# Kernel optimization log

Hardware: AMD Instinct MI355X
Metric: run time of the kernel (lower is better)

Reference implementation:

```python
import jax, jax.numpy as jnp
import numpy as np

N_NODES = 10000
N_EDGES = 160000
IN_CH = 1030
HID = 256
HEADS = 4
OUT_CH = 49
NEG_SLOPE = 0.2
EPS = 1e-5


def setup_inputs() -> dict:
    key = jax.random.key(0)
    ks = jax.random.split(key, 20)
    HC = HID * HEADS  # 1024
    inp = {
        "x": jax.random.normal(ks[0], (N_NODES, IN_CH), dtype=jnp.float32),
        "edge_index": jax.random.randint(ks[1], (2, N_EDGES), 0, N_NODES, dtype=jnp.int64),
        # conv1 (GATv2): lin_l (source), lin_r (target), att, out bias
        "c1_wl": jax.random.normal(ks[2], (IN_CH, HC), dtype=jnp.float32) * 0.03,
        "c1_bl": jnp.zeros((HC,), dtype=jnp.float32),
        "c1_wr": jax.random.normal(ks[3], (IN_CH, HC), dtype=jnp.float32) * 0.03,
        "c1_br": jnp.zeros((HC,), dtype=jnp.float32),
        "c1_att": jax.random.normal(ks[4], (HEADS, HID), dtype=jnp.float32) * 0.06,
        "c1_bias": jnp.zeros((HC,), dtype=jnp.float32),
        # norm1 (per-node LayerNorm over channels)
        "ln1_w": jnp.ones((HC,), dtype=jnp.float32),
        "ln1_b": jnp.zeros((HC,), dtype=jnp.float32),
        # conv2
        "c2_wl": jax.random.normal(ks[5], (HC, HC), dtype=jnp.float32) * 0.03,
        "c2_bl": jnp.zeros((HC,), dtype=jnp.float32),
        "c2_wr": jax.random.normal(ks[6], (HC, HC), dtype=jnp.float32) * 0.03,
        "c2_br": jnp.zeros((HC,), dtype=jnp.float32),
        "c2_att": jax.random.normal(ks[7], (HEADS, HID), dtype=jnp.float32) * 0.06,
        "c2_bias": jnp.zeros((HC,), dtype=jnp.float32),
        # norm2
        "ln2_w": jnp.ones((HC,), dtype=jnp.float32),
        "ln2_b": jnp.zeros((HC,), dtype=jnp.float32),
        # classifier: Linear(HC, HID) -> ELU -> Linear(HID, OUT_CH)
        "cls_w1": jax.random.normal(ks[8], (HC, HID), dtype=jnp.float32) * 0.03,
        "cls_b1": jnp.zeros((HID,), dtype=jnp.float32),
        "cls_w2": jax.random.normal(ks[9], (HID, OUT_CH), dtype=jnp.float32) * 0.06,
        "cls_b2": jnp.zeros((OUT_CH,), dtype=jnp.float32),
    }
    return inp


def gatv2_conv(x, src, dst, wl, bl, wr, br, att, bias, n_nodes):
    """PyG GATv2Conv, concat heads. src/dst include self loops."""
    H, C = att.shape
    xl = (x @ wl + bl).reshape(-1, H, C)  # source transform [N,H,C]
    xr = (x @ wr + br).reshape(-1, H, C)  # target transform [N,H,C]
    m = xl[src] + xr[dst]                  # [E,H,C] gather + add
    e = jnp.einsum("ehc,hc->eh", jax.nn.leaky_relu(m, NEG_SLOPE), att)  # [E,H]
    # segment softmax over destination node
    emax = jax.ops.segment_max(e, dst, num_segments=n_nodes)
    p = jnp.exp(e - emax[dst])
    denom = jax.ops.segment_sum(p, dst, num_segments=n_nodes)
    alpha = p / (denom[dst] + 1e-16)       # [E,H]
    out = jax.ops.segment_sum(xl[src] * alpha[:, :, None], dst, num_segments=n_nodes)
    return out.reshape(n_nodes, H * C) + bias


def layer_norm(x, w, b):
    mu = jnp.mean(x, axis=-1, keepdims=True)
    var = jnp.var(x, axis=-1, keepdims=True)
    return (x - mu) / jnp.sqrt(var + EPS) * w + b


def reference(x, edge_index, c1_wl, c1_bl, c1_wr, c1_br, c1_att, c1_bias,
              ln1_w, ln1_b, c2_wl, c2_bl, c2_wr, c2_br, c2_att, c2_bias,
              ln2_w, ln2_b, cls_w1, cls_b1, cls_w2, cls_b2):
    n = x.shape[0]
    loops = jnp.arange(n, dtype=edge_index.dtype)
    src = jnp.concatenate([edge_index[0], loops])  # add_self_loops=True
    dst = jnp.concatenate([edge_index[1], loops])

    h = gatv2_conv(x, src, dst, c1_wl, c1_bl, c1_wr, c1_br, c1_att, c1_bias, n)
    h = jax.nn.elu(layer_norm(h, ln1_w, ln1_b))
    # dropout: identity at inference
    h = gatv2_conv(h, src, dst, c2_wl, c2_bl, c2_wr, c2_br, c2_att, c2_bias, n)
    h = jax.nn.elu(layer_norm(h, ln2_w, ln2_b))
    h = jax.nn.elu(h @ cls_w1 + cls_b1)
    return h @ cls_w2 + cls_b2  # [N, 49]
```

## Files before the change

### kernel.cpp

```cpp
#include <hip/hip_runtime.h>
#include <stdint.h>

#define N_NODES 10000
#define N_EDGES 160000
#define E_TOT   170000
#define IN_CH   1030
#define HC      1024
#define OUT_CH  49
#define NEG_SLOPE 0.2f
#define LN_EPS 1e-5f
#define LOG2E 1.4426950408889634f

#define MPAD  10112
#define K1PAD 1088

typedef __attribute__((ext_vector_type(8))) __bf16 bf16x8;
typedef __attribute__((ext_vector_type(8))) _Float16 h8;
typedef __attribute__((ext_vector_type(4))) float floatx4;
typedef __attribute__((ext_vector_type(2))) float floatx2;
typedef _Float16 h2 __attribute__((ext_vector_type(2)));

static __device__ __forceinline__ unsigned short f2bf(float f) {
  union { float f; uint32_t u; } v; v.f = f;
  uint32_t u = v.u;
  u += 0x7fffu + ((u >> 16) & 1u);
  return (unsigned short)(u >> 16);
}
static __device__ __forceinline__ unsigned short f2h(float f) {
  _Float16 h = (_Float16)f;
  union { _Float16 h; unsigned short u; } v; v.h = h; return v.u;
}
static __device__ __forceinline__ h2 bits2h2(uint32_t u) {
  union { uint32_t i; h2 h; } v; v.i = u; return v.h;
}
static __device__ __forceinline__ floatx2 h2f2(h2 a) {
  floatx2 r; r.x = (float)a.x; r.y = (float)a.y; return r;
}

static __device__ __forceinline__ float wred_add(float x) {
#define DPP_ADD(ctrl, rmask)                                                   \
  x += __builtin_bit_cast(float, __builtin_amdgcn_update_dpp(                  \
           0, __builtin_bit_cast(int, x), ctrl, rmask, 0xf, true))
  DPP_ADD(0x111, 0xf);
  DPP_ADD(0x112, 0xf);
  DPP_ADD(0x114, 0xf);
  DPP_ADD(0x118, 0xf);
  DPP_ADD(0x142, 0xa);
  DPP_ADD(0x143, 0xc);
#undef DPP_ADD
  return __builtin_bit_cast(float,
      __builtin_amdgcn_readlane(__builtin_bit_cast(int, x), 63));
}


__global__ void cast_x_kernel(const float* __restrict__ x, unsigned short* __restrict__ xa,
                              int* __restrict__ counts) {
  int idx = blockIdx.x * 256 + threadIdx.x;
  if (idx < N_NODES) counts[idx] = 0;
  if (idx >= N_NODES * (K1PAD / 4)) return;
  int m = idx / (K1PAD / 4), k4 = idx - m * (K1PAD / 4);
  int k = k4 * 4;
  ushort4 o;
  if (k + 3 < IN_CH) {
    float2 v0 = *(const float2*)(x + (size_t)m * IN_CH + k);
    float2 v1 = *(const float2*)(x + (size_t)m * IN_CH + k + 2);
    o.x = f2bf(v0.x); o.y = f2bf(v0.y); o.z = f2bf(v1.x); o.w = f2bf(v1.y);
  } else {
    o.x = (k     < IN_CH) ? f2bf(x[(size_t)m * IN_CH + k    ]) : (unsigned short)0;
    o.y = (k + 1 < IN_CH) ? f2bf(x[(size_t)m * IN_CH + k + 1]) : (unsigned short)0;
    o.z = (k + 2 < IN_CH) ? f2bf(x[(size_t)m * IN_CH + k + 2]) : (unsigned short)0;
    o.w = (unsigned short)0;
  }
  *(ushort4*)(xa + (size_t)m * K1PAD + k) = o;
}

static __device__ __forceinline__ void transpose_body(
    float (*tile)[33], const float* __restrict__ wa, const float* __restrict__ wb,
    int split, int lda, int ldb, int Kvalid, int Kout,
    unsigned short* __restrict__ out, int bx, int by, int t, bool f16o) {
  int n0 = bx * 32, k0 = by * 32;
  int tx = t & 31, ty = t >> 5;
#pragma unroll
  for (int i = 0; i < 4; i++) {
    int k = k0 + ty + i * 8;
    int n = n0 + tx;
    float v = 0.f;
    if (k < Kvalid) {
      if (n < split) v = wa[(size_t)k * lda + n];
      else if (ldb)  v = wb[(size_t)k * ldb + (n - split)];
    }
    tile[ty + i * 8][tx] = v;
  }
  __syncthreads();
#pragma unroll
  for (int i = 0; i < 4; i++) {
    int n = n0 + ty + i * 8;
    int k = k0 + tx;
    float v = tile[tx][ty + i * 8];
    out[(size_t)n * Kout + k] = f16o ? f2h(v) : f2bf(v);
  }
}

#define NB_W1 2176
#define NB_W2 2048
#define NB_WC 256
#define NB_WC2 16
#define NB_CNT 665
__global__ __launch_bounds__(256) void prep2_kernel(
    const float* __restrict__ c1_wl, const float* __restrict__ c1_wr,
    const float* __restrict__ c2_wl, const float* __restrict__ c2_wr,
    const float* __restrict__ cls_w1, const float* __restrict__ cls_w2,
    const int* __restrict__ dstArr, int* __restrict__ counts,
    unsigned short* __restrict__ wt1, unsigned short* __restrict__ wt2,
    unsigned short* __restrict__ wtc1, unsigned short* __restrict__ wtc2)
{
  __shared__ float tile[32][33];
  int b = blockIdx.x, t = threadIdx.x;
  if (b < NB_W1) {
    transpose_body(tile, c1_wl, c1_wr, 1024, 1024, 1024, IN_CH, K1PAD, wt1, b & 63, b >> 6, t, false);
  } else if (b < NB_W1 + NB_W2) {
    int bb = b - NB_W1;
    transpose_body(tile, c2_wl, c2_wr, 1024, 1024, 1024, 1024, 1024, wt2, bb & 63, bb >> 6, t, false);
  } else if (b < NB_W1 + NB_W2 + NB_WC) {
    int bb = b - (NB_W1 + NB_W2);
    transpose_body(tile, cls_w1, cls_w1, 256, 256, 256, 1024, 1024, wtc1, bb & 7, bb >> 3, t, false);
  } else if (b < NB_W1 + NB_W2 + NB_WC + NB_WC2) {
    int bb = b - (NB_W1 + NB_W2 + NB_WC);
    transpose_body(tile, cls_w2, cls_w2, OUT_CH, OUT_CH, 0, 256, 256, wtc2, bb & 1, bb >> 1, t, true);
  } else {
    int e = (b - (NB_W1 + NB_W2 + NB_WC + NB_WC2)) * 256 + t;
    if (e < E_TOT) {
      int d = (e < N_EDGES) ? dstArr[e] : (e - N_EDGES);
      atomicAdd(&counts[d], 1);
    }
  }
}

__global__ __launch_bounds__(256) void scan_kernel(const int* __restrict__ counts,
                                                   int* __restrict__ rstart,
                                                   int* __restrict__ rwork) {
  __shared__ int sm[256];
  int t = threadIdx.x;
  int b0 = t * 40;
  int b1 = b0 + 40; if (b1 > N_NODES) b1 = N_NODES; if (b0 > N_NODES) b0 = N_NODES;
  int s = 0;
  for (int i = b0; i < b1; i++) s += counts[i];
  sm[t] = s; __syncthreads();
  for (int st = 1; st < 256; st <<= 1) {
    int add = (t >= st) ? sm[t - st] : 0;
    __syncthreads();
    sm[t] += add;
    __syncthreads();
  }
  int run = sm[t] - s;
  for (int i = b0; i < b1; i++) { rstart[i] = run; rwork[i] = run; run += counts[i]; }
  if (t == 255) rstart[N_NODES] = run;
}

__global__ void scatter_kernel(const int* __restrict__ srcArr, const int* __restrict__ dstArr,
                               int* __restrict__ rwork, int* __restrict__ csrsrc) {
  int e = blockIdx.x * 256 + threadIdx.x;
  if (e >= E_TOT) return;
  if (e < 16) csrsrc[E_TOT + e] = 0;
  int d, sv;
  if (e < N_EDGES) { d = dstArr[e]; sv = srcArr[e]; }
  else { d = e - N_EDGES; sv = d; }
  int pos = atomicAdd(&rwork[d], 1);
  csrsrc[pos] = sv;
}

template <int MODE, int KC>
__global__ __launch_bounds__(256, 4) void gemm_bf16(
    const unsigned short* __restrict__ A, const unsigned short* __restrict__ Bt,
    float* __restrict__ Cf, unsigned short* __restrict__ Cb,
    const float* __restrict__ blo, const float* __restrict__ bhi,
    int M, int ldc, int bsplit)
{
  __shared__ __align__(16) unsigned short As[128 * 64];
  __shared__ __align__(16) unsigned short Bs[128 * 64];
  const int t = threadIdx.x;
  const int w = t >> 6, lane = t & 63;

  const unsigned int nwg = gridDim.x * gridDim.y;
  const unsigned int bid = blockIdx.y * gridDim.x + blockIdx.x;
  const unsigned int q8 = nwg >> 3, r8 = nwg & 7;
  const unsigned int xcd = bid & 7, sub = bid >> 3;
  const unsigned int wg = (xcd < r8 ? xcd * (q8 + 1) : r8 * (q8 + 1) + (xcd - r8) * q8) + sub;
  const int tile_n = (wg % gridDim.x) * 128, tile_m = (wg / gridDim.x) * 128;

  floatx4 acc[4][4] = {};

  const int qq = w * 64 + lane;
  const int row0 = qq >> 3;
  const int gj = (qq & 7) ^ (row0 & 7);
  const unsigned short* gA0 = A  + (size_t)(tile_m + row0) * KC + gj * 8;
  const unsigned short* gB0 = Bt + (size_t)(tile_n + row0) * KC + gj * 8;

  const int wm = (w >> 1) * 64, wn = (w & 1) * 64;
  const int lrow = lane & 15, cg0 = (lane >> 4);
  const int sw = lrow & 7;

#pragma unroll 1
  for (int k0 = 0; k0 < KC; k0 += 64) {
#pragma unroll
    for (int p = 0; p < 4; p++) {
      __builtin_amdgcn_global_load_lds(
          (const __attribute__((address_space(1))) void*)(gA0 + p * 32 * KC),
          (__attribute__((address_space(3))) void*)(As + p * 2048 + w * 512), 16, 0, 0);
      __builtin_amdgcn_global_load_lds(
          (const __attribute__((address_space(1))) void*)(gB0 + p * 32 * KC),
          (__attribute__((address_space(3))) void*)(Bs + p * 2048 + w * 512), 16, 0, 0);
    }
    gA0 += 64; gB0 += 64;
    __syncthreads();
#pragma unroll
    for (int h = 0; h < 2; h++) {
      const int sc = (h * 4 + cg0) ^ sw;
      bf16x8 a[4], b[4];
#pragma unroll
      for (int mi = 0; mi < 4; mi++)
        a[mi] = *(const bf16x8*)(As + (wm + mi * 16 + lrow) * 64 + sc * 8);
#pragma unroll
      for (int ni = 0; ni < 4; ni++)
        b[ni] = *(const bf16x8*)(Bs + (wn + ni * 16 + lrow) * 64 + sc * 8);
#pragma unroll
      for (int mi = 0; mi < 4; mi++)
#pragma unroll
        for (int ni = 0; ni < 4; ni++)
          acc[mi][ni] = __builtin_amdgcn_mfma_f32_16x16x32_bf16(a[mi], b[ni], acc[mi][ni], 0, 0, 0);
    }
    __syncthreads();
  }

  float bcol[4];
#pragma unroll
  for (int ni = 0; ni < 4; ni++) {
    int n = tile_n + wn + ni * 16 + lrow;
    bcol[ni] = (n < bsplit) ? blo[n] : bhi[n - bsplit];
  }

  const int rbase = (lane >> 4) * 4;
#pragma unroll
  for (int mi = 0; mi < 4; mi++) {
#pragma unroll
    for (int r = 0; r < 4; r++) {
      int m = tile_m + wm + mi * 16 + rbase + r;
      if (m >= M) continue;
#pragma unroll
      for (int ni = 0; ni < 4; ni++) {
        int n = tile_n + wn + ni * 16 + lrow;
        float v = acc[mi][ni][r] + bcol[ni];
        if (MODE == 0) {
          Cf[(size_t)m * ldc + n] = v;
        } else if (MODE == 1) {
          Cf[(size_t)m * ldc + n] = v > 0.f ? v : expm1f(v);
        } else {
          Cb[(size_t)m * 2048 + n] = f2h(v);
        }
      }
    }
  }
}


__global__ __launch_bounds__(256) void gat_ln_kernel(
    const unsigned short* __restrict__ xlr,
    const float* __restrict__ att,
    const int* __restrict__ csrsrc, const int* __restrict__ rstart,
    const float* __restrict__ bias,
    const float* __restrict__ lnw, const float* __restrict__ lnb,
    unsigned short* __restrict__ out)
{
  const int d = blockIdx.x;
  const int t = threadIdx.x;
  const int lane = t & 63, wv = t >> 6;
  const int c = wv * 256 + lane * 4;

  uint2 xru = *(const uint2*)(xlr + (size_t)d * 2048 + 1024 + c);
  h2 xr0 = bits2h2(xru.x), xr1 = bits2h2(xru.y);
  float4 aw4 = *(const float4*)(att + c);
  h2 aw0, aw1;
  aw0.x = (_Float16)(aw4.x * LOG2E); aw0.y = (_Float16)(aw4.y * LOG2E);
  aw1.x = (_Float16)(aw4.z * LOG2E); aw1.y = (_Float16)(aw4.w * LOG2E);
  const h2 ns = {(_Float16)NEG_SLOPE, (_Float16)NEG_SLOPE};
  const unsigned short* xbase = xlr + c;

  int start = rstart[d], deg = rstart[d + 1] - start;

  float m = -3.0e38f, l = 0.f;
  floatx2 accA = {0.f, 0.f}, accB = {0.f, 0.f};

  int i = 0;
  if (deg >= 4) {
    int sA0 = csrsrc[start],     sA1 = csrsrc[start + 1];
    int sA2 = csrsrc[start + 2], sA3 = csrsrc[start + 3];
    uint2 uA0 = *(const uint2*)(xbase + (size_t)sA0 * 2048);
    uint2 uA1 = *(const uint2*)(xbase + (size_t)sA1 * 2048);
    uint2 uA2 = *(const uint2*)(xbase + (size_t)sA2 * 2048);
    uint2 uA3 = *(const uint2*)(xbase + (size_t)sA3 * 2048);
    int sB0 = csrsrc[start + 4], sB1 = csrsrc[start + 5];
    int sB2 = csrsrc[start + 6], sB3 = csrsrc[start + 7];
    for (; i + 4 <= deg; i += 4) {
      int sC0 = csrsrc[start + i + 8],  sC1 = csrsrc[start + i + 9];
      int sC2 = csrsrc[start + i + 10], sC3 = csrsrc[start + i + 11];
      uint2 uB0 = *(const uint2*)(xbase + (size_t)sB0 * 2048);
      uint2 uB1 = *(const uint2*)(xbase + (size_t)sB1 * 2048);
      uint2 uB2 = *(const uint2*)(xbase + (size_t)sB2 * 2048);
      uint2 uB3 = *(const uint2*)(xbase + (size_t)sB3 * 2048);

      h2 xh0a = bits2h2(uA0.x), xh0b = bits2h2(uA0.y);
      h2 xh1a = bits2h2(uA1.x), xh1b = bits2h2(uA1.y);
      h2 xh2a = bits2h2(uA2.x), xh2b = bits2h2(uA2.y);
      h2 xh3a = bits2h2(uA3.x), xh3b = bits2h2(uA3.y);
      h2 t0a = xh0a + xr0, t0b = xh0b + xr1;
      h2 t1a = xh1a + xr0, t1b = xh1b + xr1;
      h2 t2a = xh2a + xr0, t2b = xh2b + xr1;
      h2 t3a = xh3a + xr0, t3b = xh3b + xr1;
      h2 r0a = __builtin_elementwise_max(t0a, t0a * ns);
      h2 r0b = __builtin_elementwise_max(t0b, t0b * ns);
      h2 r1a = __builtin_elementwise_max(t1a, t1a * ns);
      h2 r1b = __builtin_elementwise_max(t1b, t1b * ns);
      h2 r2a = __builtin_elementwise_max(t2a, t2a * ns);
      h2 r2b = __builtin_elementwise_max(t2b, t2b * ns);
      h2 r3a = __builtin_elementwise_max(t3a, t3a * ns);
      h2 r3b = __builtin_elementwise_max(t3b, t3b * ns);
      float p0 = __builtin_amdgcn_fdot2(r0b, aw1, __builtin_amdgcn_fdot2(r0a, aw0, 0.f, false), false);
      float p1 = __builtin_amdgcn_fdot2(r1b, aw1, __builtin_amdgcn_fdot2(r1a, aw0, 0.f, false), false);
      float p2 = __builtin_amdgcn_fdot2(r2b, aw1, __builtin_amdgcn_fdot2(r2a, aw0, 0.f, false), false);
      float p3 = __builtin_amdgcn_fdot2(r3b, aw1, __builtin_amdgcn_fdot2(r3a, aw0, 0.f, false), false);
      p0 = wred_add(p0);
      p1 = wred_add(p1);
      p2 = wred_add(p2);
      p3 = wred_add(p3);
      float mx = fmaxf(fmaxf(p0, p1), fmaxf(p2, p3));
      if (mx > m) {
        float sc = exp2f(m - mx);
        floatx2 scv; scv.x = sc; scv.y = sc;
        accA *= scv; accB *= scv; l *= sc;
        m = mx;
      }
      float pe0 = exp2f(p0 - m), pe1 = exp2f(p1 - m);
      float pe2 = exp2f(p2 - m), pe3 = exp2f(p3 - m);
      floatx2 x0A = h2f2(xh0a), x0B = h2f2(xh0b);
      floatx2 x1A = h2f2(xh1a), x1B = h2f2(xh1b);
      floatx2 x2A = h2f2(xh2a), x2B = h2f2(xh2b);
      floatx2 x3A = h2f2(xh3a), x3B = h2f2(xh3b);
      floatx2 v0; v0.x = pe0; v0.y = pe0;
      floatx2 v1; v1.x = pe1; v1.y = pe1;
      floatx2 v2; v2.x = pe2; v2.y = pe2;
      floatx2 v3; v3.x = pe3; v3.y = pe3;
      accA += x0A * v0; accA += x1A * v1; accA += x2A * v2; accA += x3A * v3;
      accB += x0B * v0; accB += x1B * v1; accB += x2B * v2; accB += x3B * v3;
      l += pe0 + pe1 + pe2 + pe3;

      uA0 = uB0; uA1 = uB1; uA2 = uB2; uA3 = uB3;
      sB0 = sC0; sB1 = sC1; sB2 = sC2; sB3 = sC3;
    }
  }
  for (; i < deg; i++) {
    int s0 = csrsrc[start + i];
    uint2 u0 = *(const uint2*)(xbase + (size_t)s0 * 2048);
    h2 xh0a = bits2h2(u0.x), xh0b = bits2h2(u0.y);
    h2 t0a = xh0a + xr0, t0b = xh0b + xr1;
    h2 r0a = __builtin_elementwise_max(t0a, t0a * ns);
    h2 r0b = __builtin_elementwise_max(t0b, t0b * ns);
    float p0 = __builtin_amdgcn_fdot2(r0b, aw1, __builtin_amdgcn_fdot2(r0a, aw0, 0.f, false), false);
    p0 = wred_add(p0);
    if (p0 > m) {
      float sc = exp2f(m - p0);
      floatx2 scv; scv.x = sc; scv.y = sc;
      accA *= scv; accB *= scv; l *= sc;
      m = p0;
    }
    float pe0 = exp2f(p0 - m);
    floatx2 x0A = h2f2(xh0a), x0B = h2f2(xh0b);
    floatx2 pe0v; pe0v.x = pe0; pe0v.y = pe0;
    accA += x0A * pe0v;
    accB += x0B * pe0v;
    l += pe0;
  }

  float rd = 1.f / (l + 1e-16f);
  float4 bv = *(const float4*)(bias + c);
  float o0 = accA.x * rd + bv.x, o1 = accA.y * rd + bv.y;
  float o2 = accB.x * rd + bv.z, o3 = accB.y * rd + bv.w;

  __shared__ float ws1[4], ws2[4];
  float s1 = o0 + o1 + o2 + o3;
  float s2 = o0 * o0 + o1 * o1 + o2 * o2 + o3 * o3;
#pragma unroll
  for (int mm = 32; mm >= 1; mm >>= 1) {
    s1 += __shfl_xor(s1, mm, 64);
    s2 += __shfl_xor(s2, mm, 64);
  }
  if (lane == 0) { ws1[wv] = s1; ws2[wv] = s2; }
  __syncthreads();
  float mean = (ws1[0] + ws1[1] + ws1[2] + ws1[3]) * (1.f / 1024.f);
  float var  = (ws2[0] + ws2[1] + ws2[2] + ws2[3]) * (1.f / 1024.f) - mean * mean;
  float rstd = rsqrtf(var + LN_EPS);
  float4 wv4 = *(const float4*)(lnw + c);
  float4 bb  = *(const float4*)(lnb + c);
  float z0 = (o0 - mean) * rstd * wv4.x + bb.x; z0 = z0 > 0.f ? z0 : expm1f(z0);
  float z1 = (o1 - mean) * rstd * wv4.y + bb.y; z1 = z1 > 0.f ? z1 : expm1f(z1);
  float z2 = (o2 - mean) * rstd * wv4.z + bb.z; z2 = z2 > 0.f ? z2 : expm1f(z2);
  float z3 = (o3 - mean) * rstd * wv4.w + bb.w; z3 = z3 > 0.f ? z3 : expm1f(z3);
  ushort4 u;
  u.x = f2bf(z0); u.y = f2bf(z1); u.z = f2bf(z2); u.w = f2bf(z3);
  *(ushort4*)(out + (size_t)d * 1024 + c) = u;
}


extern __shared__ unsigned short clssm[];

__global__ __launch_bounds__(256) void cls_fused_kernel(
    const unsigned short* __restrict__ A,
    const unsigned short* __restrict__ Bt,
    const float* __restrict__ b1,
    const unsigned short* __restrict__ w2t,
    const float* __restrict__ b2,
    float* __restrict__ out)
{
  unsigned short* As = clssm;
  unsigned short* Bs = clssm + 8192;
  unsigned short* hbuf = clssm;

  const int t = threadIdx.x;
  const int w = t >> 6, lane = t & 63;
  const int tile_m = blockIdx.x * 128;

  const int q = w * 64 + lane;
  const int row0 = q >> 3;
  const int gj = (q & 7) ^ (row0 & 7);
  const unsigned short* gA0 = A  + (size_t)(tile_m + row0) * 1024 + gj * 8;
  const unsigned short* gB0 = Bt + (size_t)row0 * 1024 + gj * 8;

  const int wm = (w >> 1) * 64, wn = (w & 1) * 128;
  const int lrow = lane & 15, cg0 = lane >> 4, sw = lrow & 7;

  floatx4 acc[4][8] = {};

#pragma unroll 1
  for (int k0 = 0; k0 < 1024; k0 += 64) {
#pragma unroll
    for (int p = 0; p < 4; p++)
      __builtin_amdgcn_global_load_lds(
          (const __attribute__((address_space(1))) void*)(gA0 + p * 32 * 1024),
          (__attribute__((address_space(3))) void*)(As + p * 2048 + w * 512), 16, 0, 0);
#pragma unroll
    for (int s = 0; s < 8; s++)
      __builtin_amdgcn_global_load_lds(
          (const __attribute__((address_space(1))) void*)(gB0 + s * 32 * 1024),
          (__attribute__((address_space(3))) void*)(Bs + s * 2048 + w * 512), 16, 0, 0);
    gA0 += 64; gB0 += 64;
    __syncthreads();
#pragma unroll
    for (int h = 0; h < 2; h++) {
      const int sc = ((h << 2) | cg0) ^ sw;
      bf16x8 a[4], b[8];
#pragma unroll
      for (int mi = 0; mi < 4; mi++) {
        int ar = wm + mi * 16 + lrow;
        a[mi] = *(const bf16x8*)(As + (ar >> 5) * 2048 + (ar & 31) * 64 + sc * 8);
      }
#pragma unroll
      for (int ni = 0; ni < 8; ni++) {
        int br = wn + ni * 16 + lrow;
        b[ni] = *(const bf16x8*)(Bs + (br >> 5) * 2048 + (br & 31) * 64 + sc * 8);
      }
#pragma unroll
      for (int mi = 0; mi < 4; mi++)
#pragma unroll
        for (int ni = 0; ni < 8; ni++)
          acc[mi][ni] = __builtin_amdgcn_mfma_f32_16x16x32_bf16(a[mi], b[ni], acc[mi][ni], 0, 0, 0);
    }
    __syncthreads();
  }

  float bcol[8];
#pragma unroll
  for (int ni = 0; ni < 8; ni++) bcol[ni] = b1[wn + ni * 16 + lrow];
  const int rbase = cg0 * 4;
#pragma unroll
  for (int mi = 0; mi < 4; mi++) {
#pragma unroll
    for (int r = 0; r < 4; r++) {
      int row = wm + mi * 16 + rbase + r;
#pragma unroll
      for (int ni = 0; ni < 8; ni++) {
        int col = wn + ni * 16 + lrow;
        float v = acc[mi][ni][r] + bcol[ni];
        v = v > 0.f ? v : expm1f(v);
        int kc = (col >> 3) ^ (row & 7);
        hbuf[row * 256 + kc * 8 + (col & 7)] = f2h(v);
      }
    }
  }
  __syncthreads();

  floatx4 acc3[2][4] = {};
#pragma unroll
  for (int kst = 0; kst < 8; kst++) {
    h8 a3[2], b3[4];
#pragma unroll
    for (int mi = 0; mi < 2; mi++) {
      int ar = w * 32 + mi * 16 + lrow;
      int kc = (kst * 4 + cg0) ^ (ar & 7);
      a3[mi] = *(const h8*)(hbuf + ar * 256 + kc * 8);
    }
#pragma unroll
    for (int ni = 0; ni < 4; ni++) {
      int br = ni * 16 + lrow;
      b3[ni] = *(const h8*)(w2t + br * 256 + kst * 32 + cg0 * 8);
    }
#pragma unroll
    for (int mi = 0; mi < 2; mi++)
#pragma unroll
      for (int ni = 0; ni < 4; ni++)
        acc3[mi][ni] = __builtin_amdgcn_mfma_f32_16x16x32_f16(a3[mi], b3[ni], acc3[mi][ni], 0, 0, 0);
  }
#pragma unroll
  for (int mi = 0; mi < 2; mi++) {
    int rb = tile_m + w * 32 + mi * 16 + rbase;
#pragma unroll
    for (int r = 0; r < 4; r++) {
      int node = rb + r;
      if (node >= N_NODES) continue;
#pragma unroll
      for (int ni = 0; ni < 4; ni++) {
        int j = ni * 16 + lrow;
        if (j < OUT_CH) out[(size_t)node * OUT_CH + j] = acc3[mi][ni][r] + b2[j];
      }
    }
  }
}


extern "C" void kernel_launch(void* const* d_in, const int* in_sizes, int n_in,
                              void* d_out, int out_size, void* d_ws, size_t ws_size,
                              hipStream_t stream)
{
  const float* x       = (const float*)d_in[0];
  const int*   ei      = (const int*)d_in[1];
  const float* c1_wl   = (const float*)d_in[2];
  const float* c1_bl   = (const float*)d_in[3];
  const float* c1_wr   = (const float*)d_in[4];
  const float* c1_br   = (const float*)d_in[5];
  const float* c1_att  = (const float*)d_in[6];
  const float* c1_bias = (const float*)d_in[7];
  const float* ln1_w   = (const float*)d_in[8];
  const float* ln1_b   = (const float*)d_in[9];
  const float* c2_wl   = (const float*)d_in[10];
  const float* c2_bl   = (const float*)d_in[11];
  const float* c2_wr   = (const float*)d_in[12];
  const float* c2_br   = (const float*)d_in[13];
  const float* c2_att  = (const float*)d_in[14];
  const float* c2_bias = (const float*)d_in[15];
  const float* ln2_w   = (const float*)d_in[16];
  const float* ln2_b   = (const float*)d_in[17];
  const float* cls_w1  = (const float*)d_in[18];
  const float* cls_b1  = (const float*)d_in[19];
  const float* cls_w2  = (const float*)d_in[20];
  const float* cls_b2  = (const float*)d_in[21];

  const int* srcArr = ei;
  const int* dstArr = ei + N_EDGES;

  char* ws = (char*)d_ws;
  size_t off = 0;
  auto alloc = [&](size_t bytes) { void* p = ws + off; off += (bytes + 255) & ~(size_t)255; return p; };
  unsigned short* xa      = (unsigned short*)alloc((size_t)MPAD * K1PAD * 2);
  unsigned short* wt1     = (unsigned short*)alloc((size_t)2048 * K1PAD * 2);
  unsigned short* wt2     = (unsigned short*)alloc((size_t)2048 * 1024 * 2);
  unsigned short* wtc1    = (unsigned short*)alloc((size_t)256 * 1024 * 2);
  unsigned short* wtc2    = (unsigned short*)alloc((size_t)64 * 256 * 2);
  unsigned short* xlr     = (unsigned short*)alloc((size_t)N_NODES * 2048 * 2);
  unsigned short* hb      = (unsigned short*)alloc((size_t)MPAD * 1024 * 2);
  int*            counts  = (int*)alloc(N_NODES * 4);
  int*            rwork   = (int*)alloc(N_NODES * 4);
  int*            rstart  = (int*)alloc((N_NODES + 1) * 4);
  int*            csrsrc  = (int*)alloc((E_TOT + 16) * 4);
  (void)in_sizes; (void)n_in; (void)out_size; (void)ws_size;

  cast_x_kernel<<<(N_NODES * (K1PAD / 4) + 255) / 256, 256, 0, stream>>>(x, xa, counts);
  prep2_kernel<<<NB_W1 + NB_W2 + NB_WC + NB_WC2 + NB_CNT, 256, 0, stream>>>(
      c1_wl, c1_wr, c2_wl, c2_wr, cls_w1, cls_w2, dstArr, counts, wt1, wt2, wtc1, wtc2);

  scan_kernel<<<1, 256, 0, stream>>>(counts, rstart, rwork);
  scatter_kernel<<<(E_TOT + 255) / 256, 256, 0, stream>>>(srcArr, dstArr, rwork, csrsrc);

  gemm_bf16<2, K1PAD><<<dim3(16, 79), 256, 0, stream>>>(xa, wt1, nullptr, xlr, c1_bl, c1_br, N_NODES, 0, 1024);
  gat_ln_kernel<<<N_NODES, 256, 0, stream>>>(xlr, c1_att, csrsrc, rstart, c1_bias, ln1_w, ln1_b, hb);

  gemm_bf16<2, 1024><<<dim3(16, 79), 256, 0, stream>>>(hb, wt2, nullptr, xlr, c2_bl, c2_br, N_NODES, 0, 1024);
  gat_ln_kernel<<<N_NODES, 256, 0, stream>>>(xlr, c2_att, csrsrc, rstart, c2_bias, ln2_w, ln2_b, hb);

  cls_fused_kernel<<<79, 256, 65536, stream>>>(hb, wtc1, cls_b1, wtc2, cls_b2, (float*)d_out);
}
```

Baseline: 450.8 us.

## Widen GEMM tile to 256x128 with 512-thread workgroups

Replaces the 128x128, 256-thread bf16 GEMM with a 256x128 tile computed by 8 waves, so each B tile loaded into LDS serves twice as many rows. The grid shrinks to 640 workgroups and uses a simplified XCD-aware remap hardcoded to 80 blocks per XCD. Padded A buffers grow to 10240 rows to cover the larger M tiles. The aim is to cut global-to-LDS traffic per MFMA, at the cost of more LDS per block and possibly lower occupancy or less balanced waves.

```diff
diff --git a/kernel.cpp b/kernel.cpp
--- a/kernel.cpp
+++ b/kernel.cpp
@@ -12,6 +12,7 @@
 #define LOG2E 1.4426950408889634f
 
 #define MPAD  10112
+#define MPAD2 10240
 #define K1PAD 1088
 
 typedef __attribute__((ext_vector_type(8))) __bf16 bf16x8;
@@ -169,60 +170,59 @@
   csrsrc[pos] = sv;
 }
 
-template <int MODE, int KC>
-__global__ __launch_bounds__(256, 4) void gemm_bf16(
-    const unsigned short* __restrict__ A, const unsigned short* __restrict__ Bt,
-    float* __restrict__ Cf, unsigned short* __restrict__ Cb,
-    const float* __restrict__ blo, const float* __restrict__ bhi,
-    int M, int ldc, int bsplit)
+
+template <int KC>
+__global__ __launch_bounds__(512, 6) void gemm_wide(
+    const unsigned short* __restrict__ A,
+    const unsigned short* __restrict__ Bt,
+    unsigned short* __restrict__ Cb,
+    const float* __restrict__ blo, const float* __restrict__ bhi, int M)
 {
-  __shared__ __align__(16) unsigned short As[128 * 64];
+  __shared__ __align__(16) unsigned short As[256 * 64];
   __shared__ __align__(16) unsigned short Bs[128 * 64];
   const int t = threadIdx.x;
   const int w = t >> 6, lane = t & 63;
 
-  const unsigned int nwg = gridDim.x * gridDim.y;
   const unsigned int bid = blockIdx.y * gridDim.x + blockIdx.x;
-  const unsigned int q8 = nwg >> 3, r8 = nwg & 7;
-  const unsigned int xcd = bid & 7, sub = bid >> 3;
-  const unsigned int wg = (xcd < r8 ? xcd * (q8 + 1) : r8 * (q8 + 1) + (xcd - r8) * q8) + sub;
-  const int tile_n = (wg % gridDim.x) * 128, tile_m = (wg / gridDim.x) * 128;
+  const unsigned int wg = (bid & 7) * 80u + (bid >> 3);
+  const int tile_n = (int)(wg & 15) * 128;
+  const int tile_m = (int)(wg >> 4) * 256;
 
   floatx4 acc[4][4] = {};
 
-  const int qq = w * 64 + lane;
-  const int row0 = qq >> 3;
-  const int gj = (qq & 7) ^ (row0 & 7);
+  const int row0 = t >> 3;
+  const int gj = (t & 7) ^ (row0 & 7);
   const unsigned short* gA0 = A  + (size_t)(tile_m + row0) * KC + gj * 8;
   const unsigned short* gB0 = Bt + (size_t)(tile_n + row0) * KC + gj * 8;
 
-  const int wm = (w >> 1) * 64, wn = (w & 1) * 64;
-  const int lrow = lane & 15, cg0 = (lane >> 4);
+  const int wmb = (w >> 1) * 4096, wnb = (w & 1) * 4096;
+  const int lrow = lane & 15, cg0 = lane >> 4;
   const int sw = lrow & 7;
 
 #pragma unroll 1
   for (int k0 = 0; k0 < KC; k0 += 64) {
 #pragma unroll
-    for (int p = 0; p < 4; p++) {
+    for (int p = 0; p < 4; p++)
       __builtin_amdgcn_global_load_lds(
-          (const __attribute__((address_space(1))) void*)(gA0 + p * 32 * KC),
-          (__attribute__((address_space(3))) void*)(As + p * 2048 + w * 512), 16, 0, 0);
+          (const __attribute__((address_space(1))) void*)(gA0 + (size_t)p * 64 * KC),
+          (__attribute__((address_space(3))) void*)(As + p * 4096 + w * 512), 16, 0, 0);
+#pragma unroll
+    for (int s = 0; s < 2; s++)
       __builtin_amdgcn_global_load_lds(
-          (const __attribute__((address_space(1))) void*)(gB0 + p * 32 * KC),
-          (__attribute__((address_space(3))) void*)(Bs + p * 2048 + w * 512), 16, 0, 0);
-    }
+          (const __attribute__((address_space(1))) void*)(gB0 + (size_t)s * 64 * KC),
+          (__attribute__((address_space(3))) void*)(Bs + s * 4096 + w * 512), 16, 0, 0);
     gA0 += 64; gB0 += 64;
     __syncthreads();
 #pragma unroll
     for (int h = 0; h < 2; h++) {
-      const int sc = (h * 4 + cg0) ^ sw;
+      const int sc = ((h << 2) | cg0) ^ sw;
       bf16x8 a[4], b[4];
 #pragma unroll
       for (int mi = 0; mi < 4; mi++)
-        a[mi] = *(const bf16x8*)(As + (wm + mi * 16 + lrow) * 64 + sc * 8);
+        a[mi] = *(const bf16x8*)(As + wmb + (mi * 16 + lrow) * 64 + sc * 8);
 #pragma unroll
       for (int ni = 0; ni < 4; ni++)
-        b[ni] = *(const bf16x8*)(Bs + (wn + ni * 16 + lrow) * 64 + sc * 8);
+        b[ni] = *(const bf16x8*)(Bs + wnb + (ni * 16 + lrow) * 64 + sc * 8);
 #pragma unroll
       for (int mi = 0; mi < 4; mi++)
 #pragma unroll
@@ -235,28 +235,20 @@
   float bcol[4];
 #pragma unroll
   for (int ni = 0; ni < 4; ni++) {
-    int n = tile_n + wn + ni * 16 + lrow;
-    bcol[ni] = (n < bsplit) ? blo[n] : bhi[n - bsplit];
-  }
-
-  const int rbase = (lane >> 4) * 4;
+    int n = tile_n + (w & 1) * 64 + ni * 16 + lrow;
+    bcol[ni] = (n < 1024) ? blo[n] : bhi[n - 1024];
+  }
+  const int rbase = cg0 * 4;
 #pragma unroll
   for (int mi = 0; mi < 4; mi++) {
 #pragma unroll
     for (int r = 0; r < 4; r++) {
-      int m = tile_m + wm + mi * 16 + rbase + r;
+      int m = tile_m + (w >> 1) * 64 + mi * 16 + rbase + r;
       if (m >= M) continue;
 #pragma unroll
       for (int ni = 0; ni < 4; ni++) {
-        int n = tile_n + wn + ni * 16 + lrow;
-        float v = acc[mi][ni][r] + bcol[ni];
-        if (MODE == 0) {
-          Cf[(size_t)m * ldc + n] = v;
-        } else if (MODE == 1) {
-          Cf[(size_t)m * ldc + n] = v > 0.f ? v : expm1f(v);
-        } else {
-          Cb[(size_t)m * 2048 + n] = f2h(v);
-        }
+        int n = tile_n + (w & 1) * 64 + ni * 16 + lrow;
+        Cb[(size_t)m * 2048 + n] = f2h(acc[mi][ni][r] + bcol[ni]);
       }
     }
   }
@@ -568,13 +560,13 @@
   char* ws = (char*)d_ws;
   size_t off = 0;
   auto alloc = [&](size_t bytes) { void* p = ws + off; off += (bytes + 255) & ~(size_t)255; return p; };
-  unsigned short* xa      = (unsigned short*)alloc((size_t)MPAD * K1PAD * 2);
+  unsigned short* xa      = (unsigned short*)alloc((size_t)MPAD2 * K1PAD * 2);
   unsigned short* wt1     = (unsigned short*)alloc((size_t)2048 * K1PAD * 2);
   unsigned short* wt2     = (unsigned short*)alloc((size_t)2048 * 1024 * 2);
   unsigned short* wtc1    = (unsigned short*)alloc((size_t)256 * 1024 * 2);
   unsigned short* wtc2    = (unsigned short*)alloc((size_t)64 * 256 * 2);
   unsigned short* xlr     = (unsigned short*)alloc((size_t)N_NODES * 2048 * 2);
-  unsigned short* hb      = (unsigned short*)alloc((size_t)MPAD * 1024 * 2);
+  unsigned short* hb      = (unsigned short*)alloc((size_t)MPAD2 * 1024 * 2);
   int*            counts  = (int*)alloc(N_NODES * 4);
   int*            rwork   = (int*)alloc(N_NODES * 4);
   int*            rstart  = (int*)alloc((N_NODES + 1) * 4);
@@ -588,10 +580,10 @@
   scan_kernel<<<1, 256, 0, stream>>>(counts, rstart, rwork);
   scatter_kernel<<<(E_TOT + 255) / 256, 256, 0, stream>>>(srcArr, dstArr, rwork, csrsrc);
 
-  gemm_bf16<2, K1PAD><<<dim3(16, 79), 256, 0, stream>>>(xa, wt1, nullptr, xlr, c1_bl, c1_br, N_NODES, 0, 1024);
+  gemm_wide<K1PAD><<<dim3(16, 40), 512, 0, stream>>>(xa, wt1, xlr, c1_bl, c1_br, N_NODES);
   gat_ln_kernel<<<N_NODES, 256, 0, stream>>>(xlr, c1_att, csrsrc, rstart, c1_bias, ln1_w, ln1_b, hb);
 
-  gemm_bf16<2, 1024><<<dim3(16, 79), 256, 0, stream>>>(hb, wt2, nullptr, xlr, c2_bl, c2_br, N_NODES, 0, 1024);
+  gemm_wide<1024><<<dim3(16, 40), 512, 0, stream>>>(hb, wt2, xlr, c2_bl, c2_br, N_NODES);
   gat_ln_kernel<<<N_NODES, 256, 0, stream>>>(xlr, c2_att, csrsrc, rstart, c2_bias, ln2_w, ln2_b, hb);
 
   cls_fused_kernel<<<79, 256, 65536, stream>>>(hb, wtc1, cls_b1, wtc2, cls_b2, (float*)d_out);
```

New measurement: 683.2 us. +51.5%, slower.
